# Optimization experiments

Measured on AMD Instinct MI355X. Metric: run time of the kernel, lower is better.

Reference implementation:

```python
import jax, jax.numpy as jnp
import numpy as np


def conv2d(x, w, b=None, pad=0):
    # x: [N,C,H,W], w: [O,I,kh,kw] (cross-correlation, matches torch conv2d)
    out = jax.lax.conv_general_dilated(
        x, w, window_strides=(1, 1), padding=[(pad, pad), (pad, pad)],
        dimension_numbers=('NCHW', 'OIHW', 'NCHW'))
    if b is not None:
        out = out + b[None, :, None, None]
    return out


def se_block(f, w1, b1, w2, b2):
    # squeeze-excite: global avg pool -> 1x1 conv -> relu -> 1x1 conv -> sigmoid
    s = jnp.mean(f, axis=(2, 3), keepdims=True)
    s = jax.nn.relu(conv2d(s, w1, b1, pad=0))
    s = jax.nn.sigmoid(conv2d(s, w2, b2, pad=0))
    return f * s


def setup_inputs() -> dict:
    key = jax.random.key(0)
    ks = jax.random.split(key, 32)
    B, C, H, W = 8, 3, 128, 128
    F_, S, K = 128, 8, 72  # features, squeeze, n basis kernels
    rn = lambda k, shp, sc=0.05: (jax.random.normal(k, shp, dtype=jnp.float32) * sc)
    return {
        'x': jax.random.normal(ks[0], (B, C, H, W), dtype=jnp.float32),
        'w_head': rn(ks[1], (F_, C, 3, 3)), 'b_head': rn(ks[2], (F_,)),
        'w_h1a': rn(ks[3], (F_, F_, 3, 3)), 'b_h1a': rn(ks[4], (F_,)),
        'w_h1b': rn(ks[5], (F_, F_, 3, 3)), 'b_h1b': rn(ks[6], (F_,)),
        'du1_w1': rn(ks[7], (S, F_, 1, 1)), 'du1_b1': rn(ks[8], (S,)),
        'du1_w2': rn(ks[9], (F_, S, 1, 1)), 'du1_b2': rn(ks[10], (F_,)),
        'w_h2a': rn(ks[11], (F_, F_, 3, 3)), 'b_h2a': rn(ks[12], (F_,)),
        'w_h2b': rn(ks[13], (F_, F_, 3, 3)), 'b_h2b': rn(ks[14], (F_,)),
        'du2_w1': rn(ks[15], (S, F_, 1, 1)), 'du2_b1': rn(ks[16], (S,)),
        'du2_w2': rn(ks[17], (F_, S, 1, 1)), 'du2_b2': rn(ks[18], (F_,)),
        'w_tail': rn(ks[19], (K, F_, 3, 3)), 'b_tail': rn(ks[20], (K,)),
        'kernel': rn(ks[21], (K, 1, 5, 5), 0.2),  # fixed 72x5x5 basis
    }


def reference(x, w_head, b_head, w_h1a, b_h1a, w_h1b, b_h1b,
              du1_w1, du1_b1, du1_w2, du1_b2,
              w_h2a, b_h2a, w_h2b, b_h2b,
              du2_w1, du2_b1, du2_w2, du2_b2,
              w_tail, b_tail, kernel):
    B, C, H, W = x.shape
    K = kernel.shape[0]
    # trunk: head -> (conv relu)x2 -> SE -> (conv relu)x2 -> SE -> tail
    f = conv2d(x, w_head, b_head, pad=1)
    f = jax.nn.relu(conv2d(f, w_h1a, b_h1a, pad=1))
    f = jax.nn.relu(conv2d(f, w_h1b, b_h1b, pad=1))
    f = se_block(f, du1_w1, du1_b1, du1_w2, du1_b2)
    f = jax.nn.relu(conv2d(f, w_h2a, b_h2a, pad=1))
    f = jax.nn.relu(conv2d(f, w_h2b, b_h2b, pad=1))
    f = se_block(f, du2_w1, du2_b1, du2_w2, du2_b2)
    wgt = conv2d(f, w_tail, b_tail, pad=1).reshape(B, 1, K, H, W)
    # dynamic filtering: apply 72 fixed 5x5 basis kernels per channel, then
    # per-pixel weighted sum over the 72 basis responses
    xp = jnp.pad(x, ((0, 0), (0, 0), (2, 2), (2, 2)), mode='reflect')
    xp = xp.reshape(B * C, 1, H + 4, W + 4)
    x_com = conv2d(xp, kernel, None, pad=0).reshape(B, C, K, H, W)
    out = jnp.sum(wgt * x_com, axis=2)  # [B,3,H,W]
    return out
```

## Files before the change

kernel.cpp:

```cpp
#include <hip/hip_runtime.h>
#include <math.h>


typedef __attribute__((ext_vector_type(8))) short bf16x8;
typedef __attribute__((ext_vector_type(4))) float f32x4;

__device__ inline float bf2f(unsigned short u) {
    unsigned v = ((unsigned)u) << 16;
    return __builtin_bit_cast(float, v);
}
__device__ inline unsigned short f2bf(float f) {
    unsigned u = __builtin_bit_cast(unsigned, f);
    u += 0x7FFF + ((u >> 16) & 1);
    return (unsigned short)(u >> 16);
}

__global__ __launch_bounds__(256) void prep(
    const float* __restrict__ x, const float* __restrict__ wh,
    const float* __restrict__ bh, unsigned short* __restrict__ fb0,
    const float* __restrict__ w0, const float* __restrict__ w1,
    const float* __restrict__ w2, const float* __restrict__ w3,
    const float* __restrict__ w4, const float* __restrict__ kern,
    unsigned short* __restrict__ t0, unsigned short* __restrict__ t1,
    unsigned short* __restrict__ t2, unsigned short* __restrict__ t3,
    unsigned short* __restrict__ t4, unsigned short* __restrict__ kb,
    float* __restrict__ meanz)
{
    __shared__ float scratch[9216];
    const int tid = threadIdx.x;
    const int bid = blockIdx.x;

    if (bid >= 2048) {
        if (bid == 2122) {
            for (int idx = tid; idx < 3072; idx += 256) {
                int lq = (idx & 31) >> 3, j = idx & 7;
                int row = idx >> 5;
                int li = row & 15, snt = row >> 4;
                int s = snt >> 1, nt = snt & 1;
                int co = s * 32 + lq * 8 + j, i = nt * 16 + li;
                float v = (co < 72 && i < 25) ? kern[co * 25 + i] : 0.f;
                kb[idx] = f2bf(v);
            }
            for (int idx = tid; idx < 2048; idx += 256) meanz[idx] = 0.f;
            return;
        }
        const float* w;
        unsigned short* t;
        int Coutp, Co, co0;
        if (bid < 2112) {
            int r = bid - 2048;
            int m = r >> 4;
            co0 = (r & 15) * 8;
            w = m == 0 ? w0 : m == 1 ? w1 : m == 2 ? w2 : w3;
            t = m == 0 ? t0 : m == 1 ? t1 : m == 2 ? t2 : t3;
            Coutp = 128; Co = 128;
        } else {
            co0 = (bid - 2112) * 8;
            w = w4; t = t4; Coutp = 80; Co = 72;
        }
        const float4* src = (const float4*)(w + (size_t)co0 * 1152);
        for (int i = tid; i < 2304; i += 256) {
            float4 v = {0.f, 0.f, 0.f, 0.f};
            int co_off = (i * 4) / 1152;
            if (co0 + co_off < Co) v = src[i];
            ((float4*)scratch)[i] = v;
        }
        __syncthreads();
        const int co = (tid >> 5) & 7, ch32 = tid & 31;
        #pragma unroll
        for (int tap = 0; tap < 9; ++tap)
            #pragma unroll
            for (int kc = 0; kc < 4; ++kc)
                t[((size_t)(tap * 4 + kc) * Coutp + co0 + co) * 32 + ch32] =
                    f2bf(scratch[(co * 128 + kc * 32 + ch32) * 9 + tap]);
        return;
    }

    float* wlds = scratch;
    float* tile = scratch + 216;
    const int bx = bid & 15, cog = (bid >> 4) & 15, b = bid >> 8;
    const int tile_y = (bx >> 2) * 32, tile_x = (bx & 3) * 32;

    if (tid < 216) {
        int co = tid & 7, rest = tid >> 3, tap = rest % 9, ci = rest / 9;
        wlds[tid] = wh[((cog * 8 + co) * 3 + ci) * 9 + tap];
    }
    for (int idx = tid; idx < 3 * 34 * 34; idx += 256) {
        int ci = idx / 1156, rem = idx - ci * 1156;
        int rr = rem / 34, c = rem - rr * 34;
        int gy = tile_y - 1 + rr, gx = tile_x - 1 + c;
        float v = 0.f;
        if ((unsigned)gy < 128u && (unsigned)gx < 128u)
            v = x[(((size_t)(b * 3 + ci)) << 14) + (gy << 7) + gx];
        tile[ci * 1156 + rem] = v;
    }
    __syncthreads();

    const int ty = tid >> 4, tx = tid & 15, py = ty * 2;
    float acc[2][2][8];
    #pragma unroll
    for (int r = 0; r < 2; ++r)
        #pragma unroll
        for (int h = 0; h < 2; ++h)
            #pragma unroll
            for (int co = 0; co < 8; ++co) acc[r][h][co] = 0.f;

    #pragma unroll
    for (int ci = 0; ci < 3; ++ci) {
        #pragma unroll
        for (int ky = 0; ky < 3; ++ky) {
            #pragma unroll
            for (int kx = 0; kx < 3; ++kx) {
                const float* wp = wlds + (ci * 9 + ky * 3 + kx) * 8;
                float i00 = tile[ci * 1156 + (py + ky) * 34 + tx + kx];
                float i01 = tile[ci * 1156 + (py + ky) * 34 + tx + 16 + kx];
                float i10 = tile[ci * 1156 + (py + 1 + ky) * 34 + tx + kx];
                float i11 = tile[ci * 1156 + (py + 1 + ky) * 34 + tx + 16 + kx];
                #pragma unroll
                for (int co = 0; co < 8; ++co) {
                    float wv = wp[co];
                    acc[0][0][co] += i00 * wv;
                    acc[0][1][co] += i01 * wv;
                    acc[1][0][co] += i10 * wv;
                    acc[1][1][co] += i11 * wv;
                }
            }
        }
    }

    #pragma unroll
    for (int r = 0; r < 2; ++r) {
        #pragma unroll
        for (int h = 0; h < 2; ++h) {
            int gy = tile_y + py + r, gx = tile_x + tx + h * 16;
            bf16x8 pv;
            #pragma unroll
            for (int co = 0; co < 8; ++co)
                pv[co] = (short)f2bf(acc[r][h][co] + bh[cog * 8 + co]);
            *(bf16x8*)(fb0 + (((((size_t)b << 14) + gy * 128 + gx)) << 7) + cog * 8) = pv;
        }
    }
}

template <int LM, int NTW, int WNSPLIT, int DOMEAN>
__global__ __launch_bounds__(256, 2) void conv_mfma(
    const unsigned short* __restrict__ in, const unsigned short* __restrict__ wT,
    size_t wstride, const float* __restrict__ bias, unsigned short* __restrict__ out,
    float* __restrict__ meanb, const float* __restrict__ x,
    const unsigned short* __restrict__ kb, float* __restrict__ outf,
    int Coutp, int Cout, int relu)
{
    __shared__ unsigned short lds[20736];
    const int tid = threadIdx.x;
    const int b = blockIdx.y;
    const int row0 = (blockIdx.x >> 3) << 4;
    const int col0 = (blockIdx.x & 7) << 4;
    const int l = tid & 63, wv = tid >> 6;
    const int li = l & 15, lq = l >> 4;
    const int m_base = WNSPLIT ? (wv >> 1) * LM : wv * LM;
    const int n_base = WNSPLIT ? (wv & 1) * NTW : 0;
    const size_t inb = ((size_t)b) << 14;
    const unsigned short* wbase = wT + (size_t)b * wstride;

    f32x4 acc[LM][NTW];
    #pragma unroll
    for (int lm = 0; lm < LM; ++lm)
        #pragma unroll
        for (int nt = 0; nt < NTW; ++nt)
            acc[lm][nt] = (f32x4){0.f, 0.f, 0.f, 0.f};

    #pragma unroll 1
    for (int half = 0; half < 2; ++half) {
        __syncthreads();
        for (int u = tid; u < 2592; u += 256) {
            int px = u >> 3, g = u & 7;
            int hr = px / 18, hc = px - hr * 18;
            int gy = row0 - 1 + hr, gx = col0 - 1 + hc;
            bf16x8 v = {0, 0, 0, 0, 0, 0, 0, 0};
            if ((unsigned)gy < 128u && (unsigned)gx < 128u)
                v = *(const bf16x8*)(in + ((inb + (gy << 7) + gx) << 7) + half * 64 + g * 8);
            int p = g ^ (px & 7);
            *(bf16x8*)(lds + px * 64 + p * 8) = v;
        }
        __syncthreads();

        auto loadB = [&](bf16x8 (&dst)[NTW], int s) {
            int tap = s >> 1, kcl = s & 1;
            const unsigned short* p = wbase +
                (size_t)(tap * 4 + half * 2 + kcl) * (Coutp * 32) +
                (n_base * 16 + li) * 32 + lq * 8;
            #pragma unroll
            for (int nt = 0; nt < NTW; ++nt)
                dst[nt] = *(const bf16x8*)(p + nt * 512);
        };
        auto compute = [&](bf16x8 (&bf)[NTW], int s) {
            int tap = s >> 1, kcl = s & 1;
            int ky = tap / 3, kx = tap - ky * 3;
            int g = kcl * 4 + lq;
            #pragma unroll
            for (int lm = 0; lm < LM; ++lm) {
                int px = (m_base + lm + ky) * 18 + li + kx;
                bf16x8 af = *(const bf16x8*)(lds + px * 64 + ((g ^ (px & 7)) * 8));
                #pragma unroll
                for (int nt = 0; nt < NTW; ++nt)
                    acc[lm][nt] = __builtin_amdgcn_mfma_f32_16x16x32_bf16(
                        af, bf[nt], acc[lm][nt], 0, 0, 0);
            }
        };

        bf16x8 bufA[NTW], bufB[NTW];
        loadB(bufA, 0);
        #pragma unroll 1
        for (int it = 0; it < 18; it += 2) {
            loadB(bufB, it + 1);
            compute(bufA, it);
            if (it + 2 < 18) loadB(bufA, it + 2);
            compute(bufB, it + 1);
        }
    }

    float bv[NTW], msum[NTW];
    #pragma unroll
    for (int nt = 0; nt < NTW; ++nt) {
        int co = (n_base + nt) * 16 + li;
        bv[nt] = (co < Cout) ? bias[co] : 0.f;
        msum[nt] = 0.f;
    }

    #pragma unroll
    for (int lm = 0; lm < LM; ++lm) {
        int row = row0 + m_base + lm;
        #pragma unroll
        for (int r = 0; r < 4; ++r) {
            int col = col0 + lq * 4 + r;
            size_t pbase = (inb + row * 128 + col) * (size_t)Coutp;
            #pragma unroll
            for (int nt = 0; nt < NTW; ++nt) {
                float v = acc[lm][nt][r] + bv[nt];
                if (relu) v = fmaxf(v, 0.f);
                if (DOMEAN) msum[nt] += v;
                out[pbase + (n_base + nt) * 16 + li] = f2bf(v);
            }
        }
    }
    if (DOMEAN) {
        #pragma unroll
        for (int nt = 0; nt < NTW; ++nt) {
            float t = msum[nt];
            t += __shfl_xor(t, 16, 64);
            t += __shfl_xor(t, 32, 64);
            if (lq == 0)
                atomicAdd(&meanb[b * 128 + (n_base + nt) * 16 + li], t);
        }
    }
}

template <int LM, int NTW, int WNSPLIT, int DOMEAN, int TAILFUSE>
__global__ __launch_bounds__(256, 2) void conv_mfma_se(
    const unsigned short* __restrict__ in, const unsigned short* __restrict__ wT,
    const float* __restrict__ bias, unsigned short* __restrict__ out,
    float* __restrict__ meanb, const float* __restrict__ se_mean,
    const float* __restrict__ sw1, const float* __restrict__ sb1,
    const float* __restrict__ sw2, const float* __restrict__ sb2,
    const float* __restrict__ x, const unsigned short* __restrict__ kb,
    float* __restrict__ outf, int Coutp, int Cout, int relu)
{
    __shared__ unsigned short lds[TAILFUSE ? 26624 : 20736];
    __shared__ float slds[136];
    const int tid = threadIdx.x;
    const int b = blockIdx.y;
    const int row0 = (blockIdx.x >> 3) << 4;
    const int col0 = (blockIdx.x & 7) << 4;
    const int l = tid & 63, wv = tid >> 6;
    const int li = l & 15, lq = l >> 4;
    const int m_base = WNSPLIT ? (wv >> 1) * LM : wv * LM;
    const int n_base = WNSPLIT ? (wv & 1) * NTW : 0;
    const size_t inb = ((size_t)b) << 14;
    const unsigned short* wbase = wT;

    {
        const int grp = tid >> 5, j = tid & 31;
        float4 wv4 = ((const float4*)(sw1 + grp * 128))[j];
        float4 mv4 = ((const float4*)(se_mean + b * 128))[j];
        float part = wv4.x * mv4.x + wv4.y * mv4.y + wv4.z * mv4.z + wv4.w * mv4.w;
        part += __shfl_xor(part, 1, 64);
        part += __shfl_xor(part, 2, 64);
        part += __shfl_xor(part, 4, 64);
        part += __shfl_xor(part, 8, 64);
        part += __shfl_xor(part, 16, 64);
        if (j == 0)
            slds[128 + grp] = fmaxf(part * (1.f / 16384.f) + sb1[grp], 0.f);
    }
    __syncthreads();
    if (tid < 128) {
        float s = sb2[tid];
        #pragma unroll
        for (int j = 0; j < 8; ++j) s += sw2[tid * 8 + j] * slds[128 + j];
        slds[tid] = 1.f / (1.f + expf(-s));
    }
    __syncthreads();

    f32x4 acc[LM][NTW];
    #pragma unroll
    for (int lm = 0; lm < LM; ++lm)
        #pragma unroll
        for (int nt = 0; nt < NTW; ++nt)
            acc[lm][nt] = (f32x4){0.f, 0.f, 0.f, 0.f};

    #pragma unroll 1
    for (int half = 0; half < 2; ++half) {
        float msc[8];
        #pragma unroll
        for (int j = 0; j < 8; ++j)
            msc[j] = slds[half * 64 + (tid & 7) * 8 + j];
        __syncthreads();
        for (int u = tid; u < 2592; u += 256) {
            int px = u >> 3, g = u & 7;
            int hr = px / 18, hc = px - hr * 18;
            int gy = row0 - 1 + hr, gx = col0 - 1 + hc;
            bf16x8 v = {0, 0, 0, 0, 0, 0, 0, 0};
            if ((unsigned)gy < 128u && (unsigned)gx < 128u)
                v = *(const bf16x8*)(in + ((inb + (gy << 7) + gx) << 7) + half * 64 + g * 8);
            #pragma unroll
            for (int j = 0; j < 8; ++j)
                v[j] = (short)f2bf(bf2f((unsigned short)v[j]) * msc[j]);
            int p = g ^ (px & 7);
            *(bf16x8*)(lds + px * 64 + p * 8) = v;
        }
        __syncthreads();

        auto loadB = [&](bf16x8 (&dst)[NTW], int s) {
            int tap = s >> 1, kcl = s & 1;
            const unsigned short* p = wbase +
                (size_t)(tap * 4 + half * 2 + kcl) * (Coutp * 32) +
                (n_base * 16 + li) * 32 + lq * 8;
            #pragma unroll
            for (int nt = 0; nt < NTW; ++nt)
                dst[nt] = *(const bf16x8*)(p + nt * 512);
        };
        auto compute = [&](bf16x8 (&bf)[NTW], int s) {
            int tap = s >> 1, kcl = s & 1;
            int ky = tap / 3, kx = tap - ky * 3;
            int g = kcl * 4 + lq;
            #pragma unroll
            for (int lm = 0; lm < LM; ++lm) {
                int px = (m_base + lm + ky) * 18 + li + kx;
                bf16x8 af = *(const bf16x8*)(lds + px * 64 + ((g ^ (px & 7)) * 8));
                #pragma unroll
                for (int nt = 0; nt < NTW; ++nt)
                    acc[lm][nt] = __builtin_amdgcn_mfma_f32_16x16x32_bf16(
                        af, bf[nt], acc[lm][nt], 0, 0, 0);
            }
        };

        bf16x8 bufA[NTW], bufB[NTW];
        loadB(bufA, 0);
        #pragma unroll 1
        for (int it = 0; it < 18; it += 2) {
            loadB(bufB, it + 1);
            compute(bufA, it);
            if (it + 2 < 18) loadB(bufA, it + 2);
            compute(bufB, it + 1);
        }
    }

    float bv[NTW], msum[NTW];
    #pragma unroll
    for (int nt = 0; nt < NTW; ++nt) {
        int co = (n_base + nt) * 16 + li;
        bv[nt] = (co < Cout) ? bias[co] : 0.f;
        msum[nt] = 0.f;
    }

    if (TAILFUSE) {
        __syncthreads();
        #pragma unroll
        for (int lm = 0; lm < LM; ++lm) {
            int rowl = m_base + lm;
            #pragma unroll
            for (int r = 0; r < 4; ++r) {
                int coll = lq * 4 + r;
                #pragma unroll
                for (int nt = 0; nt < NTW; ++nt)
                    lds[(rowl * 16 + coll) * 104 + nt * 16 + li] =
                        f2bf(acc[lm][nt][r] + bv[nt]);
            }
        }
        {
            bf16x8 z = {0, 0, 0, 0, 0, 0, 0, 0};
            *(bf16x8*)(lds + tid * 104 + 80) = z;
            *(bf16x8*)(lds + tid * 104 + 88) = z;
        }
        __syncthreads();

        f32x4 eacc[4][2];
        #pragma unroll
        for (int mm = 0; mm < 4; ++mm)
            #pragma unroll
            for (int nt = 0; nt < 2; ++nt)
                eacc[mm][nt] = (f32x4){0.f, 0.f, 0.f, 0.f};
        #pragma unroll
        for (int s = 0; s < 3; ++s) {
            bf16x8 kbf[2];
            #pragma unroll
            for (int nt = 0; nt < 2; ++nt)
                kbf[nt] = *(const bf16x8*)(kb + ((s * 2 + nt) * 16 + li) * 32 + lq * 8);
            #pragma unroll
            for (int mm = 0; mm < 4; ++mm) {
                int px = (wv * 4 + mm) * 16 + li;
                bf16x8 pf = *(const bf16x8*)(lds + px * 104 + s * 32 + lq * 8);
                #pragma unroll
                for (int nt = 0; nt < 2; ++nt)
                    eacc[mm][nt] = __builtin_amdgcn_mfma_f32_16x16x32_bf16(
                        pf, kbf[nt], eacc[mm][nt], 0, 0, 0);
            }
        }
        __syncthreads();

        float* elds = (float*)lds;
        #pragma unroll
        for (int mm = 0; mm < 4; ++mm) {
            #pragma unroll
            for (int nt = 0; nt < 2; ++nt) {
                int i = nt * 16 + li;
                if (i < 25) {
                    #pragma unroll
                    for (int r = 0; r < 4; ++r) {
                        int px = (wv * 4 + mm) * 16 + lq * 4 + r;
                        elds[px * 33 + i] = eacc[mm][nt][r];
                    }
                }
            }
        }
        __syncthreads();

        const int h = row0 + (tid >> 4), w = col0 + (tid & 15);
        const int pix = h * 128 + w;
        float e[25];
        #pragma unroll
        for (int i = 0; i < 25; ++i) e[i] = elds[tid * 33 + i];

        int yy[5], xx[5];
        #pragma unroll
        for (int d = 0; d < 5; ++d) {
            int y = h - 2 + d;
            yy[d] = y < 0 ? -y : (y > 127 ? 254 - y : y);
            int xv = w - 2 + d;
            xx[d] = xv < 0 ? -xv : (xv > 127 ? 254 - xv : xv);
        }
        #pragma unroll
        for (int c = 0; c < 3; ++c) {
            const float* xc = x + ((size_t)(b * 3 + c) << 14);
            float s = 0.f;
            #pragma unroll
            for (int dy = 0; dy < 5; ++dy)
                #pragma unroll
                for (int dx = 0; dx < 5; ++dx)
                    s += e[dy * 5 + dx] * xc[yy[dy] * 128 + xx[dx]];
            outf[((size_t)(b * 3 + c) << 14) + pix] = s;
        }
        return;
    }

    #pragma unroll
    for (int lm = 0; lm < LM; ++lm) {
        int row = row0 + m_base + lm;
        #pragma unroll
        for (int r = 0; r < 4; ++r) {
            int col = col0 + lq * 4 + r;
            size_t pbase = (inb + row * 128 + col) * (size_t)Coutp;
            #pragma unroll
            for (int nt = 0; nt < NTW; ++nt) {
                float v = acc[lm][nt][r] + bv[nt];
                if (relu) v = fmaxf(v, 0.f);
                if (DOMEAN) msum[nt] += v;
                out[pbase + (n_base + nt) * 16 + li] = f2bf(v);
            }
        }
    }
    if (DOMEAN) {
        #pragma unroll
        for (int nt = 0; nt < NTW; ++nt) {
            float t = msum[nt];
            t += __shfl_xor(t, 16, 64);
            t += __shfl_xor(t, 32, 64);
            if (lq == 0)
                atomicAdd(&meanb[b * 128 + (n_base + nt) * 16 + li], t);
        }
    }
}

extern "C" void kernel_launch(void* const* d_in, const int* in_sizes, int n_in,
                              void* d_out, int out_size, void* d_ws, size_t ws_size,
                              hipStream_t stream)
{
    const float* x      = (const float*)d_in[0];
    const float* w_head = (const float*)d_in[1];
    const float* b_head = (const float*)d_in[2];
    const float* w_h1a  = (const float*)d_in[3];
    const float* b_h1a  = (const float*)d_in[4];
    const float* w_h1b  = (const float*)d_in[5];
    const float* b_h1b  = (const float*)d_in[6];
    const float* du1_w1 = (const float*)d_in[7];
    const float* du1_b1 = (const float*)d_in[8];
    const float* du1_w2 = (const float*)d_in[9];
    const float* du1_b2 = (const float*)d_in[10];
    const float* w_h2a  = (const float*)d_in[11];
    const float* b_h2a  = (const float*)d_in[12];
    const float* w_h2b  = (const float*)d_in[13];
    const float* b_h2b  = (const float*)d_in[14];
    const float* du2_w1 = (const float*)d_in[15];
    const float* du2_b1 = (const float*)d_in[16];
    const float* du2_w2 = (const float*)d_in[17];
    const float* du2_b2 = (const float*)d_in[18];
    const float* w_tail = (const float*)d_in[19];
    const float* b_tail = (const float*)d_in[20];
    const float* kern   = (const float*)d_in[21];
    float* out = (float*)d_out;

    unsigned short* fb0  = (unsigned short*)d_ws;
    unsigned short* fb1  = fb0 + 16777216;
    unsigned short* wt1  = fb1 + 16777216;
    unsigned short* wt2  = wt1 + 147456;
    unsigned short* wt3  = wt2 + 147456;
    unsigned short* wt4  = wt3 + 147456;
    unsigned short* wtt  = wt4 + 147456;
    unsigned short* kbb  = wtt + 92160;
    float* mean1  = (float*)(kbb + 3072);
    float* mean2  = mean1 + 1024;

    dim3 blk(256);
    prep<<<dim3(2123), blk, 0, stream>>>(x, w_head, b_head, fb0,
                                         w_h1a, w_h1b, w_h2a, w_h2b, w_tail,
                                         kern, wt1, wt2, wt3, wt4, wtt, kbb,
                                         mean1);

    dim3 cgrid(64, 8);
    conv_mfma<8, 4, 1, 0><<<cgrid, blk, 0, stream>>>(
        fb0, wt1, 0, b_h1a, fb1, nullptr, nullptr, nullptr, nullptr, 128, 128, 1);
    conv_mfma<8, 4, 1, 1><<<cgrid, blk, 0, stream>>>(
        fb1, wt2, 0, b_h1b, fb0, mean1, nullptr, nullptr, nullptr, 128, 128, 1);

    conv_mfma_se<8, 4, 1, 0, 0><<<cgrid, blk, 0, stream>>>(
        fb0, wt3, b_h2a, fb1, nullptr, mean1, du1_w1, du1_b1, du1_w2, du1_b2,
        nullptr, nullptr, nullptr, 128, 128, 1);
    conv_mfma<8, 4, 1, 1><<<cgrid, blk, 0, stream>>>(
        fb1, wt4, 0, b_h2b, fb0, mean2, nullptr, nullptr, nullptr, 128, 128, 1);

    conv_mfma_se<4, 5, 0, 0, 1><<<cgrid, blk, 0, stream>>>(
        fb0, wtt, b_tail, nullptr, nullptr, mean2, du2_w1, du2_b1, du2_w2,
        du2_b2, x, kbb, out, 80, 72, 0);
}
```

Baseline: 320.4 us.

## Fuse all stages into one persistent megakernel with software grid barriers

```diff
diff --git a/kernel.cpp b/kernel.cpp
--- a/kernel.cpp
+++ b/kernel.cpp
@@ -15,70 +15,28 @@
     return (unsigned short)(u >> 16);
 }
 
-__global__ __launch_bounds__(256) void prep(
+__device__ inline void grid_barrier(unsigned* ctr) {
+    __syncthreads();
+    if (threadIdx.x == 0) {
+        __threadfence();
+        atomicAdd(ctr, 1u);
+        while (__hip_atomic_load(ctr, __ATOMIC_RELAXED,
+                                 __HIP_MEMORY_SCOPE_AGENT) < 512u)
+            __builtin_amdgcn_s_sleep(2);
+        __threadfence();
+    }
+    __syncthreads();
+}
+
+__device__ void head_unit(float* scratch, int u,
     const float* __restrict__ x, const float* __restrict__ wh,
-    const float* __restrict__ bh, unsigned short* __restrict__ fb0,
-    const float* __restrict__ w0, const float* __restrict__ w1,
-    const float* __restrict__ w2, const float* __restrict__ w3,
-    const float* __restrict__ w4, const float* __restrict__ kern,
-    unsigned short* __restrict__ t0, unsigned short* __restrict__ t1,
-    unsigned short* __restrict__ t2, unsigned short* __restrict__ t3,
-    unsigned short* __restrict__ t4, unsigned short* __restrict__ kb,
-    float* __restrict__ meanz)
-{
-    __shared__ float scratch[9216];
-    const int tid = threadIdx.x;
-    const int bid = blockIdx.x;
-
-    if (bid >= 2048) {
-        if (bid == 2122) {
-            for (int idx = tid; idx < 3072; idx += 256) {
-                int lq = (idx & 31) >> 3, j = idx & 7;
-                int row = idx >> 5;
-                int li = row & 15, snt = row >> 4;
-                int s = snt >> 1, nt = snt & 1;
-                int co = s * 32 + lq * 8 + j, i = nt * 16 + li;
-                float v = (co < 72 && i < 25) ? kern[co * 25 + i] : 0.f;
-                kb[idx] = f2bf(v);
-            }
-            for (int idx = tid; idx < 2048; idx += 256) meanz[idx] = 0.f;
-            return;
-        }
-        const float* w;
-        unsigned short* t;
-        int Coutp, Co, co0;
-        if (bid < 2112) {
-            int r = bid - 2048;
-            int m = r >> 4;
-            co0 = (r & 15) * 8;
-            w = m == 0 ? w0 : m == 1 ? w1 : m == 2 ? w2 : w3;
-            t = m == 0 ? t0 : m == 1 ? t1 : m == 2 ? t2 : t3;
-            Coutp = 128; Co = 128;
-        } else {
-            co0 = (bid - 2112) * 8;
-            w = w4; t = t4; Coutp = 80; Co = 72;
-        }
-        const float4* src = (const float4*)(w + (size_t)co0 * 1152);
-        for (int i = tid; i < 2304; i += 256) {
-            float4 v = {0.f, 0.f, 0.f, 0.f};
-            int co_off = (i * 4) / 1152;
-            if (co0 + co_off < Co) v = src[i];
-            ((float4*)scratch)[i] = v;
-        }
-        __syncthreads();
-        const int co = (tid >> 5) & 7, ch32 = tid & 31;
-        #pragma unroll
-        for (int tap = 0; tap < 9; ++tap)
-            #pragma unroll
-            for (int kc = 0; kc < 4; ++kc)
-                t[((size_t)(tap * 4 + kc) * Coutp + co0 + co) * 32 + ch32] =
-                    f2bf(scratch[(co * 128 + kc * 32 + ch32) * 9 + tap]);
-        return;
-    }
-
+    const float* __restrict__ bh, unsigned short* __restrict__ fb0)
+{
+    __syncthreads();
     float* wlds = scratch;
     float* tile = scratch + 216;
-    const int bx = bid & 15, cog = (bid >> 4) & 15, b = bid >> 8;
+    const int tid = threadIdx.x;
+    const int bx = u & 15, cog = (u >> 4) & 15, b = u >> 8;
     const int tile_y = (bx >> 2) * 32, tile_x = (bx & 3) * 32;
 
     if (tid < 216) {
@@ -142,19 +100,72 @@
     }
 }
 
+__device__ void wtrans_unit(float* scratch, int r,
+    const float* __restrict__ w0, const float* __restrict__ w1,
+    const float* __restrict__ w2, const float* __restrict__ w3,
+    const float* __restrict__ w4,
+    unsigned short* __restrict__ t0, unsigned short* __restrict__ t1,
+    unsigned short* __restrict__ t2, unsigned short* __restrict__ t3,
+    unsigned short* __restrict__ t4)
+{
+    __syncthreads();
+    const int tid = threadIdx.x;
+    const float* w;
+    unsigned short* t;
+    int Coutp, Co, co0;
+    if (r < 64) {
+        int m = r >> 4;
+        co0 = (r & 15) * 8;
+        w = m == 0 ? w0 : m == 1 ? w1 : m == 2 ? w2 : w3;
+        t = m == 0 ? t0 : m == 1 ? t1 : m == 2 ? t2 : t3;
+        Coutp = 128; Co = 128;
+    } else {
+        co0 = (r - 64) * 8;
+        w = w4; t = t4; Coutp = 80; Co = 72;
+    }
+    const float4* src = (const float4*)(w + (size_t)co0 * 1152);
+    for (int i = tid; i < 2304; i += 256) {
+        float4 v = {0.f, 0.f, 0.f, 0.f};
+        int co_off = (i * 4) / 1152;
+        if (co0 + co_off < Co) v = src[i];
+        ((float4*)scratch)[i] = v;
+    }
+    __syncthreads();
+    const int co = (tid >> 5) & 7, ch32 = tid & 31;
+    #pragma unroll
+    for (int tap = 0; tap < 9; ++tap)
+        #pragma unroll
+        for (int kc = 0; kc < 4; ++kc)
+            t[((size_t)(tap * 4 + kc) * Coutp + co0 + co) * 32 + ch32] =
+                f2bf(scratch[(co * 128 + kc * 32 + ch32) * 9 + tap]);
+}
+
+__device__ void kb_meanz_unit(const float* __restrict__ kern,
+    unsigned short* __restrict__ kb, float* __restrict__ meanz)
+{
+    const int tid = threadIdx.x;
+    for (int idx = tid; idx < 3072; idx += 256) {
+        int lq = (idx & 31) >> 3, j = idx & 7;
+        int row = idx >> 5;
+        int li = row & 15, snt = row >> 4;
+        int s = snt >> 1, nt = snt & 1;
+        int co = s * 32 + lq * 8 + j, i = nt * 16 + li;
+        float v = (co < 72 && i < 25) ? kern[co * 25 + i] : 0.f;
+        kb[idx] = f2bf(v);
+    }
+    for (int idx = tid; idx < 2048; idx += 256) meanz[idx] = 0.f;
+}
+
 template <int LM, int NTW, int WNSPLIT, int DOMEAN>
-__global__ __launch_bounds__(256, 2) void conv_mfma(
+__device__ __noinline__ void conv_body(
+    unsigned short* lds, int tile, int b,
     const unsigned short* __restrict__ in, const unsigned short* __restrict__ wT,
     size_t wstride, const float* __restrict__ bias, unsigned short* __restrict__ out,
-    float* __restrict__ meanb, const float* __restrict__ x,
-    const unsigned short* __restrict__ kb, float* __restrict__ outf,
-    int Coutp, int Cout, int relu)
-{
-    __shared__ unsigned short lds[20736];
+    float* __restrict__ meanb, int Coutp, int Cout, int relu)
+{
     const int tid = threadIdx.x;
-    const int b = blockIdx.y;
-    const int row0 = (blockIdx.x >> 3) << 4;
-    const int col0 = (blockIdx.x & 7) << 4;
+    const int row0 = (tile >> 3) << 4;
+    const int col0 = (tile & 7) << 4;
     const int l = tid & 63, wv = tid >> 6;
     const int li = l & 15, lq = l >> 4;
     const int m_base = WNSPLIT ? (wv >> 1) * LM : wv * LM;
@@ -255,22 +266,20 @@
     }
 }
 
-template <int LM, int NTW, int WNSPLIT, int DOMEAN, int TAILFUSE>
-__global__ __launch_bounds__(256, 2) void conv_mfma_se(
+template <int LM, int NTW, int WNSPLIT, int TAILFUSE>
+__device__ __noinline__ void conv_se_body(
+    unsigned short* lds, float* slds, int tile, int b,
     const unsigned short* __restrict__ in, const unsigned short* __restrict__ wT,
     const float* __restrict__ bias, unsigned short* __restrict__ out,
-    float* __restrict__ meanb, const float* __restrict__ se_mean,
+    const float* __restrict__ se_mean,
     const float* __restrict__ sw1, const float* __restrict__ sb1,
     const float* __restrict__ sw2, const float* __restrict__ sb2,
     const float* __restrict__ x, const unsigned short* __restrict__ kb,
     float* __restrict__ outf, int Coutp, int Cout, int relu)
 {
-    __shared__ unsigned short lds[TAILFUSE ? 26624 : 20736];
-    __shared__ float slds[136];
     const int tid = threadIdx.x;
-    const int b = blockIdx.y;
-    const int row0 = (blockIdx.x >> 3) << 4;
-    const int col0 = (blockIdx.x & 7) << 4;
+    const int row0 = (tile >> 3) << 4;
+    const int col0 = (tile & 7) << 4;
     const int l = tid & 63, wv = tid >> 6;
     const int li = l & 15, lq = l >> 4;
     const int m_base = WNSPLIT ? (wv >> 1) * LM : wv * LM;
@@ -364,12 +373,11 @@
         }
     }
 
-    float bv[NTW], msum[NTW];
+    float bv[NTW];
     #pragma unroll
     for (int nt = 0; nt < NTW; ++nt) {
         int co = (n_base + nt) * 16 + li;
         bv[nt] = (co < Cout) ? bias[co] : 0.f;
-        msum[nt] = 0.f;
     }
 
     if (TAILFUSE) {
@@ -473,21 +481,58 @@
             for (int nt = 0; nt < NTW; ++nt) {
                 float v = acc[lm][nt][r] + bv[nt];
                 if (relu) v = fmaxf(v, 0.f);
-                if (DOMEAN) msum[nt] += v;
                 out[pbase + (n_base + nt) * 16 + li] = f2bf(v);
             }
         }
     }
-    if (DOMEAN) {
-        #pragma unroll
-        for (int nt = 0; nt < NTW; ++nt) {
-            float t = msum[nt];
-            t += __shfl_xor(t, 16, 64);
-            t += __shfl_xor(t, 32, 64);
-            if (lq == 0)
-                atomicAdd(&meanb[b * 128 + (n_base + nt) * 16 + li], t);
-        }
-    }
+}
+
+__global__ __launch_bounds__(256, 2) void mega(
+    const float* x, const float* wh, const float* bh,
+    const float* w0, const float* w1, const float* w2, const float* w3,
+    const float* w4, const float* kern,
+    const float* b_h1a, const float* b_h1b, const float* b_h2a,
+    const float* b_h2b, const float* b_tail,
+    const float* du1_w1, const float* du1_b1, const float* du1_w2,
+    const float* du1_b2, const float* du2_w1, const float* du2_b1,
+    const float* du2_w2, const float* du2_b2,
+    float* out, unsigned short* fb0, unsigned short* fb1,
+    unsigned short* wt1, unsigned short* wt2, unsigned short* wt3,
+    unsigned short* wt4, unsigned short* wtt, unsigned short* kbb,
+    float* mean1, unsigned* bars)
+{
+    __shared__ unsigned short smem[26624];
+    __shared__ float slds[136];
+    const int bid = blockIdx.x;
+    float* scratch = (float*)smem;
+    float* mean2 = mean1 + 1024;
+
+    #pragma unroll 1
+    for (int i = 0; i < 4; ++i)
+        head_unit(scratch, bid * 4 + i, x, wh, bh, fb0);
+    if (bid >= 437) {
+        int r = bid - 437;
+        if (r < 74)
+            wtrans_unit(scratch, r, w0, w1, w2, w3, w4, wt1, wt2, wt3, wt4, wtt);
+        else
+            kb_meanz_unit(kern, kbb, mean1);
+    }
+    grid_barrier(bars + 0);
+
+    const int tile = bid & 63, b = bid >> 6;
+    conv_body<8, 4, 1, 0>(smem, tile, b, fb0, wt1, 0, b_h1a, fb1, nullptr, 128, 128, 1);
+    grid_barrier(bars + 1);
+    conv_body<8, 4, 1, 1>(smem, tile, b, fb1, wt2, 0, b_h1b, fb0, mean1, 128, 128, 1);
+    grid_barrier(bars + 2);
+    conv_se_body<8, 4, 1, 0>(smem, slds, tile, b, fb0, wt3, b_h2a, fb1,
+                             mean1, du1_w1, du1_b1, du1_w2, du1_b2,
+                             nullptr, nullptr, nullptr, 128, 128, 1);
+    grid_barrier(bars + 3);
+    conv_body<8, 4, 1, 1>(smem, tile, b, fb1, wt4, 0, b_h2b, fb0, mean2, 128, 128, 1);
+    grid_barrier(bars + 4);
+    conv_se_body<4, 5, 0, 1>(smem, slds, tile, b, fb0, wtt, b_tail, nullptr,
+                             mean2, du2_w1, du2_b1, du2_w2, du2_b2,
+                             x, kbb, out, 80, 72, 0);
 }
 
 extern "C" void kernel_launch(void* const* d_in, const int* in_sizes, int n_in,
@@ -528,26 +573,13 @@
     unsigned short* kbb  = wtt + 92160;
     float* mean1  = (float*)(kbb + 3072);
     float* mean2  = mean1 + 1024;
-
-    dim3 blk(256);
-    prep<<<dim3(2123), blk, 0, stream>>>(x, w_head, b_head, fb0,
-                                         w_h1a, w_h1b, w_h2a, w_h2b, w_tail,
-                                         kern, wt1, wt2, wt3, wt4, wtt, kbb,
-                                         mean1);
-
-    dim3 cgrid(64, 8);
-    conv_mfma<8, 4, 1, 0><<<cgrid, blk, 0, stream>>>(
-        fb0, wt1, 0, b_h1a, fb1, nullptr, nullptr, nullptr, nullptr, 128, 128, 1);
-    conv_mfma<8, 4, 1, 1><<<cgrid, blk, 0, stream>>>(
-        fb1, wt2, 0, b_h1b, fb0, mean1, nullptr, nullptr, nullptr, 128, 128, 1);
-
-    conv_mfma_se<8, 4, 1, 0, 0><<<cgrid, blk, 0, stream>>>(
-        fb0, wt3, b_h2a, fb1, nullptr, mean1, du1_w1, du1_b1, du1_w2, du1_b2,
-        nullptr, nullptr, nullptr, 128, 128, 1);
-    conv_mfma<8, 4, 1, 1><<<cgrid, blk, 0, stream>>>(
-        fb1, wt4, 0, b_h2b, fb0, mean2, nullptr, nullptr, nullptr, 128, 128, 1);
-
-    conv_mfma_se<4, 5, 0, 0, 1><<<cgrid, blk, 0, stream>>>(
-        fb0, wtt, b_tail, nullptr, nullptr, mean2, du2_w1, du2_b1, du2_w2,
-        du2_b2, x, kbb, out, 80, 72, 0);
-}
+    unsigned* bars = (unsigned*)(mean2 + 1024);
+
+    hipMemsetAsync((void*)bars, 0, 8 * sizeof(unsigned), stream);
+
+    mega<<<dim3(512), dim3(256), 0, stream>>>(
+        x, w_head, b_head, w_h1a, w_h1b, w_h2a, w_h2b, w_tail, kern,
+        b_h1a, b_h1b, b_h2a, b_h2b, b_tail,
+        du1_w1, du1_b1, du1_w2, du1_b2, du2_w1, du2_b1, du2_w2, du2_b2,
+        out, fb0, fb1, wt1, wt2, wt3, wt4, wtt, kbb, mean1, bars);
+}
```

Result: slower. 675.4 us (+110.8%).

## Switch plain 128-channel convs to 32x32x16 MFMA tiles with new LDS swizzle

Applied to the files above, without the earlier changes.

```diff
diff --git a/kernel.cpp b/kernel.cpp
--- a/kernel.cpp
+++ b/kernel.cpp
@@ -4,6 +4,7 @@
 
 typedef __attribute__((ext_vector_type(8))) short bf16x8;
 typedef __attribute__((ext_vector_type(4))) float f32x4;
+typedef __attribute__((ext_vector_type(16))) float f32x16;
 
 __device__ inline float bf2f(unsigned short u) {
     unsigned v = ((unsigned)u) << 16;
@@ -142,13 +143,11 @@
     }
 }
 
-template <int LM, int NTW, int WNSPLIT, int DOMEAN>
-__global__ __launch_bounds__(256, 2) void conv_mfma(
+template <int DOMEAN>
+__global__ __launch_bounds__(256, 2) void conv_mfma32(
     const unsigned short* __restrict__ in, const unsigned short* __restrict__ wT,
-    size_t wstride, const float* __restrict__ bias, unsigned short* __restrict__ out,
-    float* __restrict__ meanb, const float* __restrict__ x,
-    const unsigned short* __restrict__ kb, float* __restrict__ outf,
-    int Coutp, int Cout, int relu)
+    const float* __restrict__ bias, unsigned short* __restrict__ out,
+    float* __restrict__ meanb, int relu)
 {
     __shared__ unsigned short lds[20736];
     const int tid = threadIdx.x;
@@ -156,18 +155,21 @@
     const int row0 = (blockIdx.x >> 3) << 4;
     const int col0 = (blockIdx.x & 7) << 4;
     const int l = tid & 63, wv = tid >> 6;
-    const int li = l & 15, lq = l >> 4;
-    const int m_base = WNSPLIT ? (wv >> 1) * LM : wv * LM;
-    const int n_base = WNSPLIT ? (wv & 1) * NTW : 0;
+    const int l5 = l >> 5;
+    const int a31 = l & 31;
+    const int rl = a31 >> 4, cl = a31 & 15;
+    const int ms = wv >> 1, ns = wv & 1;
     const size_t inb = ((size_t)b) << 14;
-    const unsigned short* wbase = wT + (size_t)b * wstride;
-
-    f32x4 acc[LM][NTW];
-    #pragma unroll
-    for (int lm = 0; lm < LM; ++lm)
-        #pragma unroll
-        for (int nt = 0; nt < NTW; ++nt)
-            acc[lm][nt] = (f32x4){0.f, 0.f, 0.f, 0.f};
+    const unsigned short* wbase = wT;
+    const int pxb = (ms * 8 + rl) * 18 + cl;
+
+    f32x16 acc[4][2];
+    #pragma unroll
+    for (int mm = 0; mm < 4; ++mm)
+        #pragma unroll
+        for (int nt = 0; nt < 2; ++nt)
+            #pragma unroll
+            for (int i = 0; i < 16; ++i) acc[mm][nt][i] = 0.f;
 
     #pragma unroll 1
     for (int half = 0; half < 2; ++half) {
@@ -179,78 +181,84 @@
             bf16x8 v = {0, 0, 0, 0, 0, 0, 0, 0};
             if ((unsigned)gy < 128u && (unsigned)gx < 128u)
                 v = *(const bf16x8*)(in + ((inb + (gy << 7) + gx) << 7) + half * 64 + g * 8);
-            int p = g ^ (px & 7);
+            int p = g ^ (px & 7) ^ (((px >> 3) & 1) << 2);
             *(bf16x8*)(lds + px * 64 + p * 8) = v;
         }
         __syncthreads();
 
-        auto loadB = [&](bf16x8 (&dst)[NTW], int s) {
-            int tap = s >> 1, kcl = s & 1;
+        auto loadB = [&](bf16x8 (&dst)[2][2], int u) {
+            int tap = u >> 1, kp = u & 1;
             const unsigned short* p = wbase +
-                (size_t)(tap * 4 + half * 2 + kcl) * (Coutp * 32) +
-                (n_base * 16 + li) * 32 + lq * 8;
-            #pragma unroll
-            for (int nt = 0; nt < NTW; ++nt)
-                dst[nt] = *(const bf16x8*)(p + nt * 512);
+                (size_t)(tap * 4 + half * 2 + kp) * (128 * 32) +
+                ((ns * 2) * 32 + a31) * 32 + l5 * 8;
+            #pragma unroll
+            for (int nt = 0; nt < 2; ++nt)
+                #pragma unroll
+                for (int k2 = 0; k2 < 2; ++k2)
+                    dst[nt][k2] = *(const bf16x8*)(p + nt * 1024 + k2 * 16);
         };
-        auto compute = [&](bf16x8 (&bf)[NTW], int s) {
-            int tap = s >> 1, kcl = s & 1;
+        auto compute = [&](bf16x8 (&bf)[2][2], int u) {
+            int tap = u >> 1, kp = u & 1;
             int ky = tap / 3, kx = tap - ky * 3;
-            int g = kcl * 4 + lq;
-            #pragma unroll
-            for (int lm = 0; lm < LM; ++lm) {
-                int px = (m_base + lm + ky) * 18 + li + kx;
-                bf16x8 af = *(const bf16x8*)(lds + px * 64 + ((g ^ (px & 7)) * 8));
-                #pragma unroll
-                for (int nt = 0; nt < NTW; ++nt)
-                    acc[lm][nt] = __builtin_amdgcn_mfma_f32_16x16x32_bf16(
-                        af, bf[nt], acc[lm][nt], 0, 0, 0);
+            int t0 = pxb + ky * 18 + kx;
+            #pragma unroll
+            for (int mm = 0; mm < 4; ++mm) {
+                int px = t0 + mm * 36;
+                int xb = (px & 7) ^ (((px >> 3) & 1) << 2);
+                #pragma unroll
+                for (int k2 = 0; k2 < 2; ++k2) {
+                    int g = kp * 4 + k2 * 2 + l5;
+                    bf16x8 af = *(const bf16x8*)(lds + px * 64 + ((g ^ xb) * 8));
+                    #pragma unroll
+                    for (int nt = 0; nt < 2; ++nt)
+                        acc[mm][nt] = __builtin_amdgcn_mfma_f32_32x32x16_bf16(
+                            af, bf[nt][k2], acc[mm][nt], 0, 0, 0);
+                }
             }
         };
 
-        bf16x8 bufA[NTW], bufB[NTW];
+        bf16x8 bufA[2][2], bufB[2][2];
         loadB(bufA, 0);
         #pragma unroll 1
-        for (int it = 0; it < 18; it += 2) {
-            loadB(bufB, it + 1);
-            compute(bufA, it);
-            if (it + 2 < 18) loadB(bufA, it + 2);
-            compute(bufB, it + 1);
-        }
-    }
-
-    float bv[NTW], msum[NTW];
-    #pragma unroll
-    for (int nt = 0; nt < NTW; ++nt) {
-        int co = (n_base + nt) * 16 + li;
-        bv[nt] = (co < Cout) ? bias[co] : 0.f;
+        for (int u = 0; u < 18; u += 2) {
+            loadB(bufB, u + 1);
+            compute(bufA, u);
+            if (u + 2 < 18) loadB(bufA, u + 2);
+            compute(bufB, u + 1);
+        }
+    }
+
+    float bv[2], msum[2];
+    #pragma unroll
+    for (int nt = 0; nt < 2; ++nt) {
+        bv[nt] = bias[(ns * 2 + nt) * 32 + a31];
         msum[nt] = 0.f;
     }
 
     #pragma unroll
-    for (int lm = 0; lm < LM; ++lm) {
-        int row = row0 + m_base + lm;
-        #pragma unroll
-        for (int r = 0; r < 4; ++r) {
-            int col = col0 + lq * 4 + r;
-            size_t pbase = (inb + row * 128 + col) * (size_t)Coutp;
-            #pragma unroll
-            for (int nt = 0; nt < NTW; ++nt) {
-                float v = acc[lm][nt][r] + bv[nt];
+    for (int mm = 0; mm < 4; ++mm) {
+        int gybase = row0 + ((ms * 4 + mm) << 1);
+        #pragma unroll
+        for (int r = 0; r < 16; ++r) {
+            int m = (r & 3) + ((r >> 2) << 3) + (l5 << 2);
+            int gy = gybase + (m >> 4), gx = col0 + (m & 15);
+            size_t pbase = (inb + (gy << 7) + gx) << 7;
+            #pragma unroll
+            for (int nt = 0; nt < 2; ++nt) {
+                float v = acc[mm][nt][r] + bv[nt];
                 if (relu) v = fmaxf(v, 0.f);
                 if (DOMEAN) msum[nt] += v;
-                out[pbase + (n_base + nt) * 16 + li] = f2bf(v);
+                out[pbase + (ns * 2 + nt) * 32 + a31] = f2bf(v);
             }
         }
     }
     if (DOMEAN) {
         #pragma unroll
-        for (int nt = 0; nt < NTW; ++nt) {
+        for (int nt = 0; nt < 2; ++nt) {
             float t = msum[nt];
-            t += __shfl_xor(t, 16, 64);
             t += __shfl_xor(t, 32, 64);
-            if (lq == 0)
-                atomicAdd(&meanb[b * 128 + (n_base + nt) * 16 + li], t);
+            if (l5 == 0)
+                atomicAdd(&meanb[b * 128 + (ns * 2 + nt) * 32 + a31], t);
         }
     }
 }
@@ -536,16 +544,13 @@
                                          mean1);
 
     dim3 cgrid(64, 8);
-    conv_mfma<8, 4, 1, 0><<<cgrid, blk, 0, stream>>>(
-        fb0, wt1, 0, b_h1a, fb1, nullptr, nullptr, nullptr, nullptr, 128, 128, 1);
-    conv_mfma<8, 4, 1, 1><<<cgrid, blk, 0, stream>>>(
-        fb1, wt2, 0, b_h1b, fb0, mean1, nullptr, nullptr, nullptr, 128, 128, 1);
+    conv_mfma32<0><<<cgrid, blk, 0, stream>>>(fb0, wt1, b_h1a, fb1, nullptr, 1);
+    conv_mfma32<1><<<cgrid, blk, 0, stream>>>(fb1, wt2, b_h1b, fb0, mean1, 1);
 
     conv_mfma_se<8, 4, 1, 0, 0><<<cgrid, blk, 0, stream>>>(
         fb0, wt3, b_h2a, fb1, nullptr, mean1, du1_w1, du1_b1, du1_w2, du1_b2,
         nullptr, nullptr, nullptr, 128, 128, 1);
-    conv_mfma<8, 4, 1, 1><<<cgrid, blk, 0, stream>>>(
-        fb1, wt4, 0, b_h2b, fb0, mean2, nullptr, nullptr, nullptr, 128, 128, 1);
+    conv_mfma32<1><<<cgrid, blk, 0, stream>>>(fb1, wt4, b_h2b, fb0, mean2, 1);
 
     conv_mfma_se<4, 5, 0, 0, 1><<<cgrid, blk, 0, stream>>>(
         fb0, wtt, b_tail, nullptr, nullptr, mean2, du2_w1, du2_b1, du2_w2,
```

Measured after the change: 335.3 us. 4.7% more time.
